# Optimization experiments

Measured on AMD Instinct MI355X. Metric: run time of the kernel, lower is better.

The kernel has to match this reference:

```python
import jax, jax.numpy as jnp
import numpy as np

D_MODEL = 1024
NUM_HEADS = 16
HEAD_DIM = D_MODEL // NUM_HEADS  # 64
ROPE_THETA = 10000.0
BATCH = 2
SEQ = 2048
NEG_INF = -1e30


def setup_inputs() -> dict:
    key = jax.random.key(0)
    ks = jax.random.split(key, 6)
    std = 1.0 / np.sqrt(D_MODEL)
    x = jax.random.normal(ks[0], (BATCH, SEQ, D_MODEL), dtype=jnp.float32)
    wq = jax.random.normal(ks[1], (D_MODEL, D_MODEL), dtype=jnp.float32) * std
    wk = jax.random.normal(ks[2], (D_MODEL, D_MODEL), dtype=jnp.float32) * std
    wv = jax.random.normal(ks[3], (D_MODEL, D_MODEL), dtype=jnp.float32) * std
    wo = jax.random.normal(ks[4], (D_MODEL, D_MODEL), dtype=jnp.float32) * std
    token_positions = jnp.broadcast_to(jnp.arange(SEQ, dtype=jnp.int32)[None, :], (BATCH, SEQ))
    return {"x": x, "token_positions": token_positions, "wq": wq, "wk": wk, "wv": wv, "wo": wo}


def _apply_rope(t, token_positions):
    # t: (B, H, S, head_dim), token_positions: (B, S)
    half = HEAD_DIM // 2
    inv_freq = 1.0 / (ROPE_THETA ** (2.0 * jnp.arange(half, dtype=jnp.float32) / HEAD_DIM))
    angles = token_positions.astype(jnp.float32)[..., None] * inv_freq  # (B, S, half)
    cos = jnp.cos(angles)[:, None, :, :]  # (B, 1, S, half)
    sin = jnp.sin(angles)[:, None, :, :]
    tp = t.reshape(*t.shape[:-1], half, 2)  # interleaved pairs
    x1, x2 = tp[..., 0], tp[..., 1]
    r1 = x1 * cos - x2 * sin
    r2 = x1 * sin + x2 * cos
    return jnp.stack([r1, r2], axis=-1).reshape(t.shape)


def reference(x, token_positions, wq, wk, wv, wo):
    B, S, D = x.shape
    H, hd = NUM_HEADS, HEAD_DIM
    # projections (Linear: y = x @ W.T, no bias)
    q = (x @ wq.T).reshape(B, S, H, hd).transpose(0, 2, 1, 3)  # (B, H, S, hd)
    k = (x @ wk.T).reshape(B, S, H, hd).transpose(0, 2, 1, 3)
    v = (x @ wv.T).reshape(B, S, H, hd).transpose(0, 2, 1, 3)
    # RoPE on Q, K
    q = _apply_rope(q, token_positions)
    k = _apply_rope(k, token_positions)
    # causal scaled dot-product attention
    scores = jnp.einsum("bhqd,bhkd->bhqk", q, k) / jnp.sqrt(jnp.float32(hd))
    mask = jnp.tril(jnp.ones((S, S), dtype=bool))
    scores = jnp.where(mask, scores, NEG_INF)
    probs = jax.nn.softmax(scores, axis=-1)
    attn = jnp.einsum("bhqk,bhkd->bhqd", probs, v)  # (B, H, S, hd)
    attn = attn.transpose(0, 2, 1, 3).reshape(B, S, D)
    return attn @ wo.T
```

## Files before the change

### kernel.cpp

```cpp
#include <hip/hip_runtime.h>
#include <stdint.h>
#include <math.h>

#define SEQ 2048
#define NH 16
#define DM 1024

typedef __bf16 bf16x8 __attribute__((ext_vector_type(8)));
typedef __bf16 bf16x2 __attribute__((ext_vector_type(2)));
typedef short s16x4 __attribute__((ext_vector_type(4)));
typedef float f32x4 __attribute__((ext_vector_type(4)));
typedef float f32x2 __attribute__((ext_vector_type(2)));

#define ASM_VMCNT0  asm volatile("s_waitcnt vmcnt(0)" ::: "memory")
#define ASM_BARRIER asm volatile("s_barrier" ::: "memory")

__device__ __forceinline__ unsigned short f2bf(float f) {
  union { float f; unsigned u; } v; v.f = f;
  unsigned r = v.u + 0x7fffu + ((v.u >> 16) & 1u);
  return (unsigned short)(r >> 16);
}
__device__ __forceinline__ unsigned pk2(float a, float b) {
  f32x2 v = {a, b};
  bf16x2 r = __builtin_convertvector(v, bf16x2);
  union { bf16x2 h; unsigned u; } c; c.h = r;
  return c.u;
}
__device__ __forceinline__ void load_lds16(const void* g, void* l) {
  __builtin_amdgcn_global_load_lds((__attribute__((address_space(1))) void*)g,
                                   (__attribute__((address_space(3))) void*)l,
                                   16, 0, 0);
}

__global__ void cvt_all(const float* __restrict__ x, const float* __restrict__ wq,
                        const float* __restrict__ wk, const float* __restrict__ wv,
                        const float* __restrict__ wo, unsigned short* __restrict__ ws) {
  const int i = blockIdx.x * blockDim.x + threadIdx.x;
  const int off = i * 4;
  const float* src;
  unsigned short* dst;
  if (off < 4194304) {
    src = x + off;  dst = ws + off;
  } else {
    const int r = off - 4194304;
    const int w = r >> 20, o = r & 1048575;
    const float* tabs[4] = {wq, wk, wv, wo};
    src = tabs[w] + o;  dst = ws + 4194304 + (w << 20) + o;
  }
  const float4 v = *(const float4*)src;
  uint2 u;
  u.x = pk2(v.x, v.y);
  u.y = pk2(v.z, v.w);
  *(uint2*)dst = u;
}

__launch_bounds__(256, 3)
__global__ void gemm_qkv(const unsigned short* __restrict__ X,
                         const unsigned short* __restrict__ W3,
                         unsigned short* __restrict__ Qr,
                         unsigned short* __restrict__ Kr,
                         unsigned short* __restrict__ Vt,
                         const int* __restrict__ tp) {
  __shared__ __align__(16) char smem[32768];

  const int t = threadIdx.x;
  const int lane = t & 63, wave = t >> 6;
  const int quad = lane >> 4, l16 = lane & 15;
  const int m0 = blockIdx.y * 128, n0 = blockIdx.x * 128;
  const int wm = (wave >> 1) * 64, wn = (wave & 1) * 64;

  f32x4 acc[4][4];
#pragma unroll
  for (int i = 0; i < 4; i++)
#pragma unroll
    for (int j = 0; j < 4; j++) { acc[i][j][0]=0.f; acc[i][j][1]=0.f; acc[i][j][2]=0.f; acc[i][j][3]=0.f; }

  const int rr = t >> 2;
  const int cc = (t & 3) * 8;

#define QKV_STAGE(bufidx, k0_) do {                                               \
    char* a_ = smem + (bufidx) * 8192;                                            \
    char* b_ = smem + 16384 + (bufidx) * 8192;                                    \
    _Pragma("unroll")                                                             \
    for (int i_ = 0; i_ < 2; i_++) {                                              \
      load_lds16(X  + (uint64_t)(m0 + i_ * 64 + rr) * 1024 + (k0_) + cc,          \
                 a_ + i_ * 4096 + wave * 1024);                                   \
      load_lds16(W3 + (uint64_t)(n0 + i_ * 64 + rr) * 1024 + (k0_) + cc,          \
                 b_ + i_ * 4096 + wave * 1024);                                   \
    }                                                                             \
  } while (0)

  QKV_STAGE(0, 0);

  for (int k0 = 0; k0 < 1024; k0 += 32) {
    const int buf = (k0 >> 5) & 1;
    ASM_VMCNT0;
    ASM_BARRIER;
    if (k0 + 32 < 1024) QKV_STAGE(buf ^ 1, k0 + 32);
    char* As = smem + buf * 8192;
    char* Bs = smem + 16384 + buf * 8192;

    bf16x8 af[4], bfr[4];
#pragma unroll
    for (int i = 0; i < 4; i++) {
      af[i]  = *(const bf16x8*)(As + (wm + i * 16 + l16) * 64 + quad * 16);
      bfr[i] = *(const bf16x8*)(Bs + (wn + i * 16 + l16) * 64 + quad * 16);
    }
#pragma unroll
    for (int i = 0; i < 4; i++)
#pragma unroll
      for (int j = 0; j < 4; j++)
        acc[i][j] = __builtin_amdgcn_mfma_f32_16x16x32_bf16(af[i], bfr[j], acc[i][j], 0, 0, 0);
  }
#undef QKV_STAGE

  if (n0 < 2048) {
    unsigned short* dst = (n0 < 1024) ? Qr : Kr;
    float fr[4]; int dd[4], hh[4];
#pragma unroll
    for (int j = 0; j < 4; j++) {
      const int n = n0 + wn + j * 16 + l16;
      dd[j] = n & 63;
      hh[j] = (n & 1023) >> 6;
      fr[j] = __builtin_amdgcn_exp2f(-0.20762050594f * (float)(dd[j] & ~1)) * 0.15915494309f;
    }
    const float sgnodd = (l16 & 1) ? 1.f : -1.f;
#pragma unroll
    for (int i = 0; i < 4; i++) {
#pragma unroll
      for (int r = 0; r < 4; r++) {
        const int m = m0 + wm + i * 16 + quad * 4 + r;
        const int s = m & 2047, b = m >> 11;
        const float posf = (float)tp[m];
#pragma unroll
        for (int j = 0; j < 4; j++) {
          const float v = acc[i][j][r];
          const float p = __shfl_xor(v, 1);
          float rev = posf * fr[j];
          rev -= floorf(rev);
          float sn, cs;
          asm("v_sin_f32 %0, %1" : "=v"(sn) : "v"(rev));
          asm("v_cos_f32 %0, %1" : "=v"(cs) : "v"(rev));
          const float rv = fmaf(v, cs, p * sn * sgnodd);
          dst[((uint64_t)((b * NH + hh[j]) * SEQ + s)) * 64 + dd[j]] = f2bf(rv);
        }
      }
    }
  } else {
#pragma unroll
    for (int i = 0; i < 4; i++) {
      const int m = m0 + wm + i * 16 + quad * 4;
      const int s = m & 2047, b = m >> 11;
#pragma unroll
      for (int j = 0; j < 4; j++) {
        const int n = n0 - 2048 + wn + j * 16 + l16;
        const int h = n >> 6, d = n & 63;
        uint2 w;
        w.x = pk2(acc[i][j][0], acc[i][j][1]);
        w.y = pk2(acc[i][j][2], acc[i][j][3]);
        *(uint2*)(Vt + ((uint64_t)((b * NH + h) * 64 + d)) * SEQ + s) = w;
      }
    }
  }
}

__launch_bounds__(256, 2)
__global__ void gemm_ao(const unsigned short* __restrict__ A,
                        const unsigned short* __restrict__ B,
                        float* __restrict__ C) {
  __shared__ __align__(16) char smem[24576];

  const int t = threadIdx.x;
  const int lane = t & 63, wave = t >> 6;
  const int quad = lane >> 4, l16 = lane & 15;
  const int m0 = blockIdx.y * 128, n0 = blockIdx.x * 64;
  const int wm = (wave >> 1) * 64, wn = (wave & 1) * 32;

  f32x4 acc[4][2];
#pragma unroll
  for (int i = 0; i < 4; i++)
#pragma unroll
    for (int j = 0; j < 2; j++) { acc[i][j][0]=0.f; acc[i][j][1]=0.f; acc[i][j][2]=0.f; acc[i][j][3]=0.f; }

  const int rr = t >> 2;
  const int cc = (t & 3) * 8;

#define AO_STAGE(bufidx, k0_) do {                                                \
    char* a_ = smem + (bufidx) * 8192;                                            \
    char* b_ = smem + 16384 + (bufidx) * 4096;                                    \
    _Pragma("unroll")                                                             \
    for (int i_ = 0; i_ < 2; i_++)                                                \
      load_lds16(A + (uint64_t)(m0 + i_ * 64 + rr) * 1024 + (k0_) + cc,           \
                 a_ + i_ * 4096 + wave * 1024);                                   \
    load_lds16(B + (uint64_t)(n0 + rr) * 1024 + (k0_) + cc, b_ + wave * 1024);    \
  } while (0)

  AO_STAGE(0, 0);

  for (int k0 = 0; k0 < 1024; k0 += 32) {
    const int buf = (k0 >> 5) & 1;
    ASM_VMCNT0;
    ASM_BARRIER;
    if (k0 + 32 < 1024) AO_STAGE(buf ^ 1, k0 + 32);
    char* As = smem + buf * 8192;
    char* Bs = smem + 16384 + buf * 4096;

    bf16x8 af[4], bfr[2];
#pragma unroll
    for (int i = 0; i < 4; i++)
      af[i] = *(const bf16x8*)(As + (wm + i * 16 + l16) * 64 + quad * 16);
#pragma unroll
    for (int j = 0; j < 2; j++)
      bfr[j] = *(const bf16x8*)(Bs + (wn + j * 16 + l16) * 64 + quad * 16);
#pragma unroll
    for (int i = 0; i < 4; i++)
#pragma unroll
      for (int j = 0; j < 2; j++)
        acc[i][j] = __builtin_amdgcn_mfma_f32_16x16x32_bf16(af[i], bfr[j], acc[i][j], 0, 0, 0);
  }
#undef AO_STAGE

#pragma unroll
  for (int i = 0; i < 4; i++)
#pragma unroll
    for (int j = 0; j < 2; j++)
#pragma unroll
      for (int r = 0; r < 4; r++) {
        const int m = m0 + wm + i * 16 + quad * 4 + r;
        const int n = n0 + wn + j * 16 + l16;
        C[(uint64_t)m * DM + n] = acc[i][j][r];
      }
}

__launch_bounds__(512, 2)
__global__ void flash_attn(const unsigned short* __restrict__ Q,
                           const unsigned short* __restrict__ K,
                           const unsigned short* __restrict__ Vt,
                           unsigned short* __restrict__ Oa) {
  __shared__ __align__(16) char smem[32768];

  const int t = threadIdx.x;
  const int lane = t & 63, wave = t >> 6;
  const int quad = lane >> 4, l16 = lane & 15;
  const int lid = blockIdx.x;
  const int bh = lid & 31;
  const int a = lid >> 5;
  const uint64_t base = (uint64_t)bh * (SEQ * 64);
  const int qb0 = a * 128, qb1 = (15 - a) * 128;
  const int n0 = 2 * a + 2;
  const int qg0 = qb0 + wave * 16 + l16;
  const int qg1 = qb1 + wave * 16 + l16;
  const int b = bh >> 4, h = bh & 15;

  bf16x8 qf0[2], qf1[2];
  {
    const unsigned short* qp = Q + base + (uint64_t)qg0 * 64 + quad * 8;
    qf0[0] = *(const bf16x8*)qp;  qf0[1] = *(const bf16x8*)(qp + 32);
    const unsigned short* qq = Q + base + (uint64_t)qg1 * 64 + quad * 8;
    qf1[0] = *(const bf16x8*)qq;  qf1[1] = *(const bf16x8*)(qq + 32);
  }

  f32x4 o[4];
#pragma unroll
  for (int i = 0; i < 4; i++) { o[i][0]=0.f; o[i][1]=0.f; o[i][2]=0.f; o[i][3]=0.f; }
  float lI = 0.f;

  const int srow = wave * 8 + (lane >> 3);
  const int sc = ((lane & 7) ^ ((lane >> 3) & 7)) * 8;
  const int swz = (l16 & 7);

#define STAGE(bufidx, kb_) do {                                                   \
    load_lds16(K  + base + (uint64_t)((kb_) + srow) * 64 + sc,                    \
               smem + (bufidx) * 8192 + wave * 1024);                             \
    load_lds16(Vt + base + (uint64_t)srow * SEQ + (kb_) + sc,                     \
               smem + 16384 + (bufidx) * 8192 + wave * 1024);                     \
  } while (0)

  STAGE(0, 0);

  const float c1 = 0.18033688011f;

  for (int it = 0; it < 34; it++) {
    const bool ph1 = it >= n0;
    const int kb = (ph1 ? it - n0 : it) * 64;
    const int buf = it & 1;
    ASM_VMCNT0;
    ASM_BARRIER;
    if (it + 1 < 34) {
      const int itn = it + 1;
      const int kbn = ((itn >= n0) ? itn - n0 : itn) * 64;
      STAGE(buf ^ 1, kbn);
    }
    char* ks = smem + buf * 8192;
    char* vs = smem + 16384 + buf * 8192;

    const bf16x8* qf = ph1 ? qf1 : qf0;
    const int qg = ph1 ? qg1 : qg0;
    const int qb = ph1 ? qb1 : qb0;
    int nbmax = ((qb + wave * 16 + 15 - kb) >> 4) + 1;
    nbmax = nbmax > 4 ? 4 : (nbmax < 0 ? 0 : nbmax);
    const bool diag = (kb + 63) > (qb + wave * 16);

    f32x4 sf[4];
    float ls = 0.f;
#pragma unroll
    for (int nb = 0; nb < 4; nb++) {
      if (nb < nbmax) {
        f32x4 s; s[0]=0.f; s[1]=0.f; s[2]=0.f; s[3]=0.f;
#pragma unroll
        for (int kk = 0; kk < 2; kk++) {
          bf16x8 kfr = *(const bf16x8*)(ks + (nb * 16 + l16) * 128 + (((kk * 4 + quad) ^ swz) * 16));
          s = __builtin_amdgcn_mfma_f32_16x16x32_bf16(kfr, qf[kk], s, 0, 0, 0);
        }
        if (diag) {
#pragma unroll
          for (int r = 0; r < 4; r++) {
            const int key = kb + nb * 16 + quad * 4 + r;
            const float p = (key <= qg) ? __builtin_amdgcn_exp2f(s[r] * c1) : 0.f;
            sf[nb][r] = p;  ls += p;
          }
        } else {
#pragma unroll
          for (int r = 0; r < 4; r++) {
            const float p = __builtin_amdgcn_exp2f(s[r] * c1);
            sf[nb][r] = p;  ls += p;
          }
        }
      }
    }
    lI += ls;

#pragma unroll
    for (int nb = 0; nb < 4; nb++) {
      if (nb < nbmax) {
        union { uint2 u; s16x4 h; } pc;
        pc.u.x = pk2(sf[nb][0], sf[nb][1]);
        pc.u.y = pk2(sf[nb][2], sf[nb][3]);
#pragma unroll
        for (int db = 0; db < 4; db++) {
          s16x4 vf = *(const s16x4*)(vs + (db * 16 + l16) * 128 +
                                     (((2 * nb + (quad >> 1)) ^ swz) * 16) + (quad & 1) * 8);
          o[db] = __builtin_amdgcn_mfma_f32_16x16x16bf16_1k(vf, pc.h, o[db], 0, 0, 0);
        }
      }
    }

    if (it == n0 - 1) {
      float lr = lI;
      lr += __shfl_xor(lr, 16);
      lr += __shfl_xor(lr, 32);
      const float invl = 1.0f / lr;
      unsigned short* orow = Oa + ((uint64_t)(b * SEQ + qg0)) * DM + h * 64 + quad * 4;
#pragma unroll
      for (int db = 0; db < 4; db++) {
        uint2 w;
        w.x = pk2(o[db][0] * invl, o[db][1] * invl);
        w.y = pk2(o[db][2] * invl, o[db][3] * invl);
        *(uint2*)(orow + db * 16) = w;
        o[db][0]=0.f; o[db][1]=0.f; o[db][2]=0.f; o[db][3]=0.f;
      }
      lI = 0.f;
    }
  }
#undef STAGE

  float lr = lI;
  lr += __shfl_xor(lr, 16);
  lr += __shfl_xor(lr, 32);
  const float invl = 1.0f / lr;
  unsigned short* orow = Oa + ((uint64_t)(b * SEQ + qg1)) * DM + h * 64 + quad * 4;
#pragma unroll
  for (int db = 0; db < 4; db++) {
    uint2 w;
    w.x = pk2(o[db][0] * invl, o[db][1] * invl);
    w.y = pk2(o[db][2] * invl, o[db][3] * invl);
    *(uint2*)(orow + db * 16) = w;
  }
}

extern "C" void kernel_launch(void* const* d_in, const int* in_sizes, int n_in,
                              void* d_out, int out_size, void* d_ws, size_t ws_size,
                              hipStream_t stream) {
  const float* x  = (const float*)d_in[0];
  const int* tp   = (const int*)d_in[1];
  const float* wq = (const float*)d_in[2];
  const float* wk = (const float*)d_in[3];
  const float* wv = (const float*)d_in[4];
  const float* wo = (const float*)d_in[5];
  float* out = (float*)d_out;

  unsigned short* ws = (unsigned short*)d_ws;
  unsigned short* xb  = ws;
  unsigned short* w3b = ws + 4194304;
  unsigned short* wob = ws + 7340032;
  unsigned short* Qr  = ws + 8388608;
  unsigned short* Kr  = ws + 12582912;
  unsigned short* Vt  = ws + 16777216;
  unsigned short* At  = ws + 20971520;

  cvt_all<<<8192, 256, 0, stream>>>(x, wq, wk, wv, wo, ws);
  gemm_qkv<<<dim3(24, 32), 256, 0, stream>>>(xb, w3b, Qr, Kr, Vt, tp);
  flash_attn<<<256, 512, 0, stream>>>(Qr, Kr, Vt, At);
  gemm_ao<<<dim3(16, 32), 256, 0, stream>>>(At, wob, out);
}
```

Before: 179.7 us.

## Permute V-transpose layout for wide LDS reads and enlarge output-projection tiles

The QKV GEMM epilogue now writes V-transposed with a permuted sequence index within each 64-key block. This lets flash attention fetch one 16-byte LDS vector per row and split it into two MFMA operands, instead of issuing two separate 8-byte reads. Separately, the output-projection GEMM tile grows from 128x64 to 128x128 with a 4x4 accumulator per wave, raising data reuse per LDS load. The cost is more registers and fewer blocks in that GEMM, plus a coupled layout contract between the two kernels.

```diff
diff --git a/kernel.cpp b/kernel.cpp
--- a/kernel.cpp
+++ b/kernel.cpp
@@ -9,6 +9,7 @@
 typedef __bf16 bf16x8 __attribute__((ext_vector_type(8)));
 typedef __bf16 bf16x2 __attribute__((ext_vector_type(2)));
 typedef short s16x4 __attribute__((ext_vector_type(4)));
+typedef short s16x8 __attribute__((ext_vector_type(8)));
 typedef float f32x4 __attribute__((ext_vector_type(4)));
 typedef float f32x2 __attribute__((ext_vector_type(2)));
 
@@ -151,6 +152,9 @@
     for (int i = 0; i < 4; i++) {
       const int m = m0 + wm + i * 16 + quad * 4;
       const int s = m & 2047, b = m >> 11;
+      const int sl = s & 63;
+      const int qv = (sl >> 2) & 3, nv = sl >> 4;
+      const int g = (s & ~63) + qv * 16 + (nv >> 1) * 8 + (nv & 1) * 4;
 #pragma unroll
       for (int j = 0; j < 4; j++) {
         const int n = n0 - 2048 + wn + j * 16 + l16;
@@ -158,7 +162,7 @@
         uint2 w;
         w.x = pk2(acc[i][j][0], acc[i][j][1]);
         w.y = pk2(acc[i][j][2], acc[i][j][3]);
-        *(uint2*)(Vt + ((uint64_t)((b * NH + h) * 64 + d)) * SEQ + s) = w;
+        *(uint2*)(Vt + ((uint64_t)((b * NH + h) * 64 + d)) * SEQ + g) = w;
       }
     }
   }
@@ -168,31 +172,33 @@
 __global__ void gemm_ao(const unsigned short* __restrict__ A,
                         const unsigned short* __restrict__ B,
                         float* __restrict__ C) {
-  __shared__ __align__(16) char smem[24576];
+  __shared__ __align__(16) char smem[32768];
 
   const int t = threadIdx.x;
   const int lane = t & 63, wave = t >> 6;
   const int quad = lane >> 4, l16 = lane & 15;
-  const int m0 = blockIdx.y * 128, n0 = blockIdx.x * 64;
-  const int wm = (wave >> 1) * 64, wn = (wave & 1) * 32;
-
-  f32x4 acc[4][2];
+  const int m0 = blockIdx.y * 128, n0 = blockIdx.x * 128;
+  const int wm = (wave >> 1) * 64, wn = (wave & 1) * 64;
+
+  f32x4 acc[4][4];
 #pragma unroll
   for (int i = 0; i < 4; i++)
 #pragma unroll
-    for (int j = 0; j < 2; j++) { acc[i][j][0]=0.f; acc[i][j][1]=0.f; acc[i][j][2]=0.f; acc[i][j][3]=0.f; }
+    for (int j = 0; j < 4; j++) { acc[i][j][0]=0.f; acc[i][j][1]=0.f; acc[i][j][2]=0.f; acc[i][j][3]=0.f; }
 
   const int rr = t >> 2;
   const int cc = (t & 3) * 8;
 
-#define AO_STAGE(bufidx, k0_) do {                                                \
+#define AO_STAGE(bufidx, k0_) do {                                               \
     char* a_ = smem + (bufidx) * 8192;                                            \
-    char* b_ = smem + 16384 + (bufidx) * 4096;                                    \
+    char* b_ = smem + 16384 + (bufidx) * 8192;                                    \
     _Pragma("unroll")                                                             \
-    for (int i_ = 0; i_ < 2; i_++)                                                \
+    for (int i_ = 0; i_ < 2; i_++) {                                              \
       load_lds16(A + (uint64_t)(m0 + i_ * 64 + rr) * 1024 + (k0_) + cc,           \
                  a_ + i_ * 4096 + wave * 1024);                                   \
-    load_lds16(B + (uint64_t)(n0 + rr) * 1024 + (k0_) + cc, b_ + wave * 1024);    \
+      load_lds16(B + (uint64_t)(n0 + i_ * 64 + rr) * 1024 + (k0_) + cc,           \
+                 b_ + i_ * 4096 + wave * 1024);                                   \
+    }                                                                             \
   } while (0)
 
   AO_STAGE(0, 0);
@@ -203,19 +209,18 @@
     ASM_BARRIER;
     if (k0 + 32 < 1024) AO_STAGE(buf ^ 1, k0 + 32);
     char* As = smem + buf * 8192;
-    char* Bs = smem + 16384 + buf * 4096;
-
-    bf16x8 af[4], bfr[2];
+    char* Bs = smem + 16384 + buf * 8192;
+
+    bf16x8 af[4], bfr[4];
+#pragma unroll
+    for (int i = 0; i < 4; i++) {
+      af[i]  = *(const bf16x8*)(As + (wm + i * 16 + l16) * 64 + quad * 16);
+      bfr[i] = *(const bf16x8*)(Bs + (wn + i * 16 + l16) * 64 + quad * 16);
+    }
 #pragma unroll
     for (int i = 0; i < 4; i++)
-      af[i] = *(const bf16x8*)(As + (wm + i * 16 + l16) * 64 + quad * 16);
-#pragma unroll
-    for (int j = 0; j < 2; j++)
-      bfr[j] = *(const bf16x8*)(Bs + (wn + j * 16 + l16) * 64 + quad * 16);
-#pragma unroll
-    for (int i = 0; i < 4; i++)
-#pragma unroll
-      for (int j = 0; j < 2; j++)
+#pragma unroll
+      for (int j = 0; j < 4; j++)
         acc[i][j] = __builtin_amdgcn_mfma_f32_16x16x32_bf16(af[i], bfr[j], acc[i][j], 0, 0, 0);
   }
 #undef AO_STAGE
@@ -223,7 +228,7 @@
 #pragma unroll
   for (int i = 0; i < 4; i++)
 #pragma unroll
-    for (int j = 0; j < 2; j++)
+    for (int j = 0; j < 4; j++)
 #pragma unroll
       for (int r = 0; r < 4; r++) {
         const int m = m0 + wm + i * 16 + quad * 4 + r;
@@ -331,16 +336,27 @@
     lI += ls;
 
 #pragma unroll
-    for (int nb = 0; nb < 4; nb++) {
-      if (nb < nbmax) {
-        union { uint2 u; s16x4 h; } pc;
-        pc.u.x = pk2(sf[nb][0], sf[nb][1]);
-        pc.u.y = pk2(sf[nb][2], sf[nb][3]);
+    for (int np = 0; np < 2; np++) {
+      if (2 * np < nbmax) {
+        union { uint2 u; s16x4 h; } p0;
+        p0.u.x = pk2(sf[2 * np][0], sf[2 * np][1]);
+        p0.u.y = pk2(sf[2 * np][2], sf[2 * np][3]);
+        const bool hi = (2 * np + 1 < nbmax);
+        union { uint2 u; s16x4 h; } p1;
+        if (hi) {
+          p1.u.x = pk2(sf[2 * np + 1][0], sf[2 * np + 1][1]);
+          p1.u.y = pk2(sf[2 * np + 1][2], sf[2 * np + 1][3]);
+        }
 #pragma unroll
         for (int db = 0; db < 4; db++) {
-          s16x4 vf = *(const s16x4*)(vs + (db * 16 + l16) * 128 +
-                                     (((2 * nb + (quad >> 1)) ^ swz) * 16) + (quad & 1) * 8);
-          o[db] = __builtin_amdgcn_mfma_f32_16x16x16bf16_1k(vf, pc.h, o[db], 0, 0, 0);
+          s16x8 vv = *(const s16x8*)(vs + (db * 16 + l16) * 128 +
+                                     (((quad * 2 + np) ^ swz) * 16));
+          s16x4 vlo = __builtin_shufflevector(vv, vv, 0, 1, 2, 3);
+          o[db] = __builtin_amdgcn_mfma_f32_16x16x16bf16_1k(vlo, p0.h, o[db], 0, 0, 0);
+          if (hi) {
+            s16x4 vhi = __builtin_shufflevector(vv, vv, 4, 5, 6, 7);
+            o[db] = __builtin_amdgcn_mfma_f32_16x16x16bf16_1k(vhi, p1.h, o[db], 0, 0, 0);
+          }
         }
       }
     }
@@ -401,5 +417,5 @@
   cvt_all<<<8192, 256, 0, stream>>>(x, wq, wk, wv, wo, ws);
   gemm_qkv<<<dim3(24, 32), 256, 0, stream>>>(xb, w3b, Qr, Kr, Vt, tp);
   flash_attn<<<256, 512, 0, stream>>>(Qr, Kr, Vt, At);
-  gemm_ao<<<dim3(16, 32), 256, 0, stream>>>(At, wob, out);
-}
+  gemm_ao<<<dim3(8, 32), 256, 0, stream>>>(At, wob, out);
+}
```

After: 179.3 us. No clear change (-0.2%).
